# Kernel optimization log

Measured on AMD Instinct MI355X. Metric: run time of the kernel, lower is better.

The kernel has to match this reference:

```python
import jax, jax.numpy as jnp
import numpy as np
from jax import lax

N = 2048
P = 256
F_J = 0.05      # sparsity of recurrent matrix J
F_OUT = 0.05    # sparsity of readout
DT = 0.1
ON_TIME = 10
T = 200


def _activation(x):
    # Tanh_shifted_and_scaled: rates in [0, 1]
    return 0.5 * (1.0 + jnp.tanh(x))


def setup_inputs() -> dict:
    key = jax.random.key(0)
    k1, k2, k3, k4, k5 = jax.random.split(key, 5)
    # patterns ~ Uniform(-1, 1), shape [N, P]
    patterns = jax.random.uniform(k1, (N, P), jnp.float32, -1.0, 1.0)
    # sparse recurrent matrix J: gaussian values, density F_J, gain g
    g = 10.0 * 0.1 ** 0.25 / np.sqrt(N * P * np.sqrt(F_J))
    J_dense = jax.random.normal(k2, (N, N), jnp.float32) * jnp.float32(g)
    mask = jax.random.uniform(k3, (N, N)) < F_J
    J = jnp.where(mask, J_dense, 0.0).astype(jnp.float32)
    # sparse readout: ones at a random F_OUT fraction of units (frozen)
    w_out = (jax.random.uniform(k4, (N,)) < F_OUT).astype(jnp.float32)
    return {"patterns": patterns, "J": J, "w_out": w_out, "N_time_steps": T}


def reference(patterns, J, w_out, N_time_steps):
    # Batched over all P patterns at once (columns of [N, P] state).
    n = patterns.shape[0]
    x0 = jnp.zeros_like(patterns)           # [N, P]
    r0 = _activation(x0)

    def step(carry, ti):
        x, rates = carry
        inp = jnp.where(ti < ON_TIME, patterns, 0.0)      # [N, P]
        x = x + DT * (-x + J @ rates + inp)               # [N, P]
        rates = _activation(x)
        out_t = w_out @ rates                             # [P]
        return (x, rates), out_t

    _, outs = lax.scan(step, (x0, r0), jnp.arange(N_time_steps))  # [T, P]
    readout = outs.T / n                                   # [P, T]
    return readout
```

## Files before the change

kernel.cpp:

```cpp
#include <hip/hip_runtime.h>
#include <hip/hip_bf16.h>


#define NN 2048
#define PP 256
#define PAD 256
#define DT_C 0.1f
#define ON_TIME_C 10

__global__ void build_ell_kernel(const float* __restrict__ J,
                                 float2* __restrict__ ell,
                                 int* __restrict__ nnz) {
    int row  = blockIdx.x * (blockDim.x >> 6) + (threadIdx.x >> 6);
    int lane = threadIdx.x & 63;
    if (row >= NN) return;
    const float* Jrow = J + (size_t)row * NN;
    int base = 0;
    for (int c = 0; c < NN / 64; ++c) {
        float f = Jrow[c * 64 + lane];
        bool nz = (f != 0.0f);
        unsigned long long m = __ballot(nz);
        int pre = __popcll(m & ((1ull << lane) - 1ull));
        int pos = base + pre;
        if (nz && pos < PAD)
            ell[(size_t)row * PAD + pos] = make_float2(f, __int_as_float(c * 64 + lane));
        base += __popcll(m);
    }
    if (lane == 0) nnz[row] = (base < PAD) ? base : PAD;
}

__global__ void init_kernel(float* __restrict__ x, float* __restrict__ r,
                            float* __restrict__ out, int nout) {
    int i = blockIdx.x * blockDim.x + threadIdx.x;
    x[i] = 0.0f;
    r[i] = 0.5f;
    if (i < nout) out[i] = 0.0f;
}

__global__ __launch_bounds__(256) void step_kernel(
    const float2* __restrict__ ell, const int* __restrict__ nnz,
    const float* __restrict__ rates_in, float* __restrict__ rates_out,
    float* __restrict__ x, const float* __restrict__ patterns,
    const float* __restrict__ w_out, float* __restrict__ out,
    int t, int T, int with_input) {
    int row  = blockIdx.x;
    int tid  = threadIdx.x;
    int w    = tid >> 6;
    int lane = tid & 63;

    __shared__ float2 s_ell[PAD];
    __shared__ float  s_part[4][PP];

    int cnt = nnz[row];
    if (tid < cnt) s_ell[tid] = ell[(size_t)row * PAD + tid];
    __syncthreads();

    const float4* rin4 = (const float4*)rates_in;
    float4 acc = make_float4(0.f, 0.f, 0.f, 0.f);
    #pragma unroll 4
    for (int k = w; k < cnt; k += 4) {
        float2 e = s_ell[k];
        int   j  = __float_as_int(e.y);
        float4 rv = rin4[j * (PP / 4) + lane];
        acc.x = fmaf(e.x, rv.x, acc.x);
        acc.y = fmaf(e.x, rv.y, acc.y);
        acc.z = fmaf(e.x, rv.z, acc.z);
        acc.w = fmaf(e.x, rv.w, acc.w);
    }
    ((float4*)s_part[w])[lane] = acc;
    __syncthreads();

    float sum = s_part[0][tid] + s_part[1][tid] + s_part[2][tid] + s_part[3][tid];

    size_t off = (size_t)row * PP + tid;
    float xv  = x[off];
    float inp = with_input ? patterns[off] : 0.0f;
    xv += DT_C * (sum + inp - xv);
    x[off] = xv;
    float r = 0.5f * (1.0f + tanhf(xv));
    rates_out[off] = r;

    if (w_out[row] != 0.0f) {
        atomicAdd(&out[(size_t)tid * T + t], r * (1.0f / (float)NN));
    }
}

extern "C" void kernel_launch(void* const* d_in, const int* in_sizes, int n_in,
                              void* d_out, int out_size, void* d_ws, size_t ws_size,
                              hipStream_t stream) {
    const float* patterns = (const float*)d_in[0];
    const float* J        = (const float*)d_in[1];
    const float* w_out    = (const float*)d_in[2];
    float* out            = (float*)d_out;

    const int T = out_size / PP;

    size_t off = 0;
    auto alloc = [&](size_t bytes) {
        void* p = (char*)d_ws + off;
        off += (bytes + 255) & ~(size_t)255;
        return p;
    };
    float2* ell  = (float2*)alloc((size_t)NN * PAD * 8);
    int*    nnz  = (int*)   alloc((size_t)NN * 4);
    float*  x    = (float*) alloc((size_t)NN * PP * 4);
    float*  r0   = (float*) alloc((size_t)NN * PP * 4);
    float*  r1   = (float*) alloc((size_t)NN * PP * 4);
    (void)ws_size; (void)n_in; (void)in_sizes;

    build_ell_kernel<<<NN / 4, 256, 0, stream>>>(J, ell, nnz);

    init_kernel<<<(NN * PP) / 256, 256, 0, stream>>>(x, r0, out, PP * T);

    for (int t = 0; t < T; ++t) {
        const float* rin = (t & 1) ? r1 : r0;
        float*      rout = (t & 1) ? r0 : r1;
        step_kernel<<<NN, PP, 0, stream>>>(ell, nnz, rin, rout, x, patterns,
                                           w_out, out, t, T,
                                           (t < ON_TIME_C) ? 1 : 0);
    }
}
```

Before: 2.353 ms.

## Assign one wavefront per row and unroll sparse gather eightfold

```diff
diff --git a/kernel.cpp b/kernel.cpp
--- a/kernel.cpp
+++ b/kernel.cpp
@@ -37,51 +37,85 @@
     if (i < nout) out[i] = 0.0f;
 }
 
-__global__ __launch_bounds__(256) void step_kernel(
+__global__ __launch_bounds__(256, 2) void step_kernel(
     const float2* __restrict__ ell, const int* __restrict__ nnz,
     const float* __restrict__ rates_in, float* __restrict__ rates_out,
     float* __restrict__ x, const float* __restrict__ patterns,
     const float* __restrict__ w_out, float* __restrict__ out,
     int t, int T, int with_input) {
-    int row  = blockIdx.x;
-    int tid  = threadIdx.x;
-    int w    = tid >> 6;
-    int lane = tid & 63;
+    int w    = threadIdx.x >> 6;
+    int lane = threadIdx.x & 63;
+    int row  = blockIdx.x * 4 + w;
 
-    __shared__ float2 s_ell[PAD];
-    __shared__ float  s_part[4][PP];
+    __shared__ float2 s_ell[4][PAD];
 
     int cnt = nnz[row];
-    if (tid < cnt) s_ell[tid] = ell[(size_t)row * PAD + tid];
-    __syncthreads();
+    const float2* erow = ell + (size_t)row * PAD;
+    for (int i = lane; i < cnt; i += 64)
+        s_ell[w][i] = erow[i];
 
     const float4* rin4 = (const float4*)rates_in;
     float4 acc = make_float4(0.f, 0.f, 0.f, 0.f);
-    #pragma unroll 4
-    for (int k = w; k < cnt; k += 4) {
-        float2 e = s_ell[k];
-        int   j  = __float_as_int(e.y);
-        float4 rv = rin4[j * (PP / 4) + lane];
+    int k = 0;
+    for (; k + 8 <= cnt; k += 8) {
+        float2 e[8];
+        float4 rv[8];
+        #pragma unroll
+        for (int u = 0; u < 8; ++u) e[u] = s_ell[w][k + u];
+        #pragma unroll
+        for (int u = 0; u < 8; ++u)
+            rv[u] = rin4[__float_as_int(e[u].y) * (PP / 4) + lane];
+        #pragma unroll
+        for (int u = 0; u < 8; ++u) {
+            acc.x = fmaf(e[u].x, rv[u].x, acc.x);
+            acc.y = fmaf(e[u].x, rv[u].y, acc.y);
+            acc.z = fmaf(e[u].x, rv[u].z, acc.z);
+            acc.w = fmaf(e[u].x, rv[u].w, acc.w);
+        }
+    }
+    for (; k < cnt; ++k) {
+        float2 e = s_ell[w][k];
+        float4 rv = rin4[__float_as_int(e.y) * (PP / 4) + lane];
         acc.x = fmaf(e.x, rv.x, acc.x);
         acc.y = fmaf(e.x, rv.y, acc.y);
         acc.z = fmaf(e.x, rv.z, acc.z);
         acc.w = fmaf(e.x, rv.w, acc.w);
     }
-    ((float4*)s_part[w])[lane] = acc;
-    __syncthreads();
 
-    float sum = s_part[0][tid] + s_part[1][tid] + s_part[2][tid] + s_part[3][tid];
+    size_t off4 = (size_t)row * (PP / 4) + lane;
+    float4* x4        = (float4*)x;
+    float4* rout4     = (float4*)rates_out;
+    const float4* p4  = (const float4*)patterns;
 
-    size_t off = (size_t)row * PP + tid;
-    float xv  = x[off];
-    float inp = with_input ? patterns[off] : 0.0f;
-    xv += DT_C * (sum + inp - xv);
-    x[off] = xv;
-    float r = 0.5f * (1.0f + tanhf(xv));
-    rates_out[off] = r;
+    float4 xv = x4[off4];
+    if (with_input) {
+        float4 pv = p4[off4];
+        xv.x += DT_C * (acc.x + pv.x - xv.x);
+        xv.y += DT_C * (acc.y + pv.y - xv.y);
+        xv.z += DT_C * (acc.z + pv.z - xv.z);
+        xv.w += DT_C * (acc.w + pv.w - xv.w);
+    } else {
+        xv.x += DT_C * (acc.x - xv.x);
+        xv.y += DT_C * (acc.y - xv.y);
+        xv.z += DT_C * (acc.z - xv.z);
+        xv.w += DT_C * (acc.w - xv.w);
+    }
+    x4[off4] = xv;
+
+    float4 r;
+    r.x = 0.5f * (1.0f + tanhf(xv.x));
+    r.y = 0.5f * (1.0f + tanhf(xv.y));
+    r.z = 0.5f * (1.0f + tanhf(xv.z));
+    r.w = 0.5f * (1.0f + tanhf(xv.w));
+    rout4[off4] = r;
 
     if (w_out[row] != 0.0f) {
-        atomicAdd(&out[(size_t)tid * T + t], r * (1.0f / (float)NN));
+        const float s = 1.0f / (float)NN;
+        int p = lane * 4;
+        atomicAdd(&out[(size_t)(p + 0) * T + t], r.x * s);
+        atomicAdd(&out[(size_t)(p + 1) * T + t], r.y * s);
+        atomicAdd(&out[(size_t)(p + 2) * T + t], r.z * s);
+        atomicAdd(&out[(size_t)(p + 3) * T + t], r.w * s);
     }
 }
 
@@ -93,7 +127,7 @@
     const float* w_out    = (const float*)d_in[2];
     float* out            = (float*)d_out;
 
-    const int T = out_size / PP;
+    int T = out_size / PP;
 
     size_t off = 0;
     auto alloc = [&](size_t bytes) {
@@ -101,22 +135,21 @@
         off += (bytes + 255) & ~(size_t)255;
         return p;
     };
-    float2* ell  = (float2*)alloc((size_t)NN * PAD * 8);
-    int*    nnz  = (int*)   alloc((size_t)NN * 4);
-    float*  x    = (float*) alloc((size_t)NN * PP * 4);
-    float*  r0   = (float*) alloc((size_t)NN * PP * 4);
-    float*  r1   = (float*) alloc((size_t)NN * PP * 4);
+    float2* ell = (float2*)alloc((size_t)NN * PAD * 8);
+    int*    nnz = (int*)   alloc((size_t)NN * 4);
+    float*  x   = (float*) alloc((size_t)NN * PP * 4);
+    float*  r0  = (float*) alloc((size_t)NN * PP * 4);
+    float*  r1  = (float*) alloc((size_t)NN * PP * 4);
     (void)ws_size; (void)n_in; (void)in_sizes;
 
     build_ell_kernel<<<NN / 4, 256, 0, stream>>>(J, ell, nnz);
-
     init_kernel<<<(NN * PP) / 256, 256, 0, stream>>>(x, r0, out, PP * T);
 
     for (int t = 0; t < T; ++t) {
         const float* rin = (t & 1) ? r1 : r0;
         float*      rout = (t & 1) ? r0 : r1;
-        step_kernel<<<NN, PP, 0, stream>>>(ell, nnz, rin, rout, x, patterns,
-                                           w_out, out, t, T,
-                                           (t < ON_TIME_C) ? 1 : 0);
+        step_kernel<<<NN / 4, 256, 0, stream>>>(ell, nnz, rin, rout, x,
+                                                patterns, w_out, out, t, T,
+                                                (t < ON_TIME_C) ? 1 : 0);
     }
 }
```

New measurement: 2.825 ms. +20.0%, slower.

## Tile sparse matmul over K-chunks with rates staged in shared memory

Applied to the files above, without the earlier changes.

```diff
diff --git a/kernel.cpp b/kernel.cpp
--- a/kernel.cpp
+++ b/kernel.cpp
@@ -7,6 +7,11 @@
 #define PAD 256
 #define DT_C 0.1f
 #define ON_TIME_C 10
+#define KT 512
+#define NT 4
+#define MB 128
+#define CT 16
+#define SR_STRIDE 5
 
 __global__ void build_ell_kernel(const float* __restrict__ J,
                                  float2* __restrict__ ell,
@@ -29,6 +34,22 @@
     if (lane == 0) nnz[row] = (base < PAD) ? base : PAD;
 }
 
+__global__ void seg_kernel(const float2* __restrict__ ell,
+                           const int* __restrict__ nnz,
+                           int* __restrict__ seg) {
+    int r = blockIdx.x * blockDim.x + threadIdx.x;
+    if (r >= NN) return;
+    int cnt = nnz[r];
+    const float2* eb = ell + (size_t)r * PAD;
+    int tt = 0;
+    seg[r * (NT + 1)] = 0;
+    for (int i = 0; i < cnt; ++i) {
+        int k = __float_as_int(eb[i].y);
+        while (k >= (tt + 1) * KT) { ++tt; seg[r * (NT + 1) + tt] = i; }
+    }
+    while (tt < NT) { ++tt; seg[r * (NT + 1) + tt] = cnt; }
+}
+
 __global__ void init_kernel(float* __restrict__ x, float* __restrict__ r,
                             float* __restrict__ out, int nout) {
     int i = blockIdx.x * blockDim.x + threadIdx.x;
@@ -37,51 +58,114 @@
     if (i < nout) out[i] = 0.0f;
 }
 
-__global__ __launch_bounds__(256) void step_kernel(
-    const float2* __restrict__ ell, const int* __restrict__ nnz,
+__global__ __launch_bounds__(512) void step_kernel(
+    const float2* __restrict__ ell, const int* __restrict__ seg,
     const float* __restrict__ rates_in, float* __restrict__ rates_out,
     float* __restrict__ x, const float* __restrict__ patterns,
     const float* __restrict__ w_out, float* __restrict__ out,
     int t, int T, int with_input) {
-    int row  = blockIdx.x;
     int tid  = threadIdx.x;
-    int w    = tid >> 6;
-    int lane = tid & 63;
-
-    __shared__ float2 s_ell[PAD];
-    __shared__ float  s_part[4][PP];
-
-    int cnt = nnz[row];
-    if (tid < cnt) s_ell[tid] = ell[(size_t)row * PAD + tid];
+    int rt   = blockIdx.x >> 4;
+    int ct   = blockIdx.x & 15;
+    int rloc = tid >> 2;
+    int cq   = tid & 3;
+    int row  = rt * MB + rloc;
+    int cb4  = ct * (CT / 4);
+
+    __shared__ float4 sr4[KT * SR_STRIDE];
+
+    const float4* rin4 = (const float4*)rates_in;
+    const float2* eb   = ell + (size_t)row * PAD;
+
+    int sg[NT + 1];
+    #pragma unroll
+    for (int i = 0; i <= NT; ++i) sg[i] = seg[row * (NT + 1) + i];
+
+    float4 acc = make_float4(0.f, 0.f, 0.f, 0.f);
+    float4 gA, gB, gC, gD;
+
+    {
+        const float4* p = rin4 + ((size_t)(0 * KT + tid) * (PP / 4) + cb4);
+        gA = p[0]; gB = p[1]; gC = p[2]; gD = p[3];
+        sr4[tid * SR_STRIDE + 0] = gA;
+        sr4[tid * SR_STRIDE + 1] = gB;
+        sr4[tid * SR_STRIDE + 2] = gC;
+        sr4[tid * SR_STRIDE + 3] = gD;
+    }
+    {
+        const float4* p = rin4 + ((size_t)(1 * KT + tid) * (PP / 4) + cb4);
+        gA = p[0]; gB = p[1]; gC = p[2]; gD = p[3];
+    }
     __syncthreads();
 
-    const float4* rin4 = (const float4*)rates_in;
-    float4 acc = make_float4(0.f, 0.f, 0.f, 0.f);
-    #pragma unroll 4
-    for (int k = w; k < cnt; k += 4) {
-        float2 e = s_ell[k];
-        int   j  = __float_as_int(e.y);
-        float4 rv = rin4[j * (PP / 4) + lane];
-        acc.x = fmaf(e.x, rv.x, acc.x);
-        acc.y = fmaf(e.x, rv.y, acc.y);
-        acc.z = fmaf(e.x, rv.z, acc.z);
-        acc.w = fmaf(e.x, rv.w, acc.w);
-    }
-    ((float4*)s_part[w])[lane] = acc;
-    __syncthreads();
-
-    float sum = s_part[0][tid] + s_part[1][tid] + s_part[2][tid] + s_part[3][tid];
-
-    size_t off = (size_t)row * PP + tid;
-    float xv  = x[off];
-    float inp = with_input ? patterns[off] : 0.0f;
-    xv += DT_C * (sum + inp - xv);
-    x[off] = xv;
-    float r = 0.5f * (1.0f + tanhf(xv));
-    rates_out[off] = r;
+    #pragma unroll
+    for (int tt = 0; tt < NT; ++tt) {
+        int s0 = sg[tt], s1 = sg[tt + 1], kb = tt * KT;
+        float2 eA[8], eB[8];
+        #pragma unroll
+        for (int u = 0; u < 8; ++u) {
+            int i = s0 + u;
+            eA[u] = (i < s1) ? eb[i] : make_float2(0.f, __int_as_float(kb));
+        }
+        for (int i0 = s0; i0 < s1; i0 += 8) {
+            #pragma unroll
+            for (int u = 0; u < 8; ++u) {
+                int i = i0 + 8 + u;
+                eB[u] = (i < s1) ? eb[i] : make_float2(0.f, __int_as_float(kb));
+            }
+            #pragma unroll
+            for (int u = 0; u < 8; ++u) {
+                int kl = __float_as_int(eA[u].y) - kb;
+                float4 rv = sr4[kl * SR_STRIDE + cq];
+                acc.x = fmaf(eA[u].x, rv.x, acc.x);
+                acc.y = fmaf(eA[u].x, rv.y, acc.y);
+                acc.z = fmaf(eA[u].x, rv.z, acc.z);
+                acc.w = fmaf(eA[u].x, rv.w, acc.w);
+            }
+            #pragma unroll
+            for (int u = 0; u < 8; ++u) eA[u] = eB[u];
+        }
+        if (tt < NT - 1) {
+            __syncthreads();
+            sr4[tid * SR_STRIDE + 0] = gA;
+            sr4[tid * SR_STRIDE + 1] = gB;
+            sr4[tid * SR_STRIDE + 2] = gC;
+            sr4[tid * SR_STRIDE + 3] = gD;
+            if (tt < NT - 2) {
+                const float4* p = rin4 + ((size_t)((tt + 2) * KT + tid) * (PP / 4) + cb4);
+                gA = p[0]; gB = p[1]; gC = p[2]; gD = p[3];
+            }
+            __syncthreads();
+        }
+    }
+
+    size_t o4 = (size_t)row * (PP / 4) + cb4 + cq;
+    float4 xv = ((const float4*)x)[o4];
+    float4 a  = acc;
+    if (with_input) {
+        float4 pv = ((const float4*)patterns)[o4];
+        a.x += pv.x; a.y += pv.y; a.z += pv.z; a.w += pv.w;
+    }
+    xv.x += DT_C * (a.x - xv.x);
+    xv.y += DT_C * (a.y - xv.y);
+    xv.z += DT_C * (a.z - xv.z);
+    xv.w += DT_C * (a.w - xv.w);
+    ((float4*)x)[o4] = xv;
+
+    float4 r4;
+    r4.x = 0.5f * (1.0f + tanhf(xv.x));
+    r4.y = 0.5f * (1.0f + tanhf(xv.y));
+    r4.z = 0.5f * (1.0f + tanhf(xv.z));
+    r4.w = 0.5f * (1.0f + tanhf(xv.w));
+    ((float4*)rates_out)[o4] = r4;
 
     if (w_out[row] != 0.0f) {
-        atomicAdd(&out[(size_t)tid * T + t], r * (1.0f / (float)NN));
+        const float s = 1.0f / (float)NN;
+        int p0 = ct * CT + cq * 4;
+        atomicAdd(&out[(size_t)(p0 + 0) * T + t], r4.x * s);
+        atomicAdd(&out[(size_t)(p0 + 1) * T + t], r4.y * s);
+        atomicAdd(&out[(size_t)(p0 + 2) * T + t], r4.z * s);
+        atomicAdd(&out[(size_t)(p0 + 3) * T + t], r4.w * s);
     }
 }
 
@@ -93,7 +177,7 @@
     const float* w_out    = (const float*)d_in[2];
     float* out            = (float*)d_out;
 
-    const int T = out_size / PP;
+    int T = out_size / PP;
 
     size_t off = 0;
     auto alloc = [&](size_t bytes) {
@@ -101,22 +185,23 @@
         off += (bytes + 255) & ~(size_t)255;
         return p;
     };
-    float2* ell  = (float2*)alloc((size_t)NN * PAD * 8);
-    int*    nnz  = (int*)   alloc((size_t)NN * 4);
-    float*  x    = (float*) alloc((size_t)NN * PP * 4);
-    float*  r0   = (float*) alloc((size_t)NN * PP * 4);
-    float*  r1   = (float*) alloc((size_t)NN * PP * 4);
+    float2* ell = (float2*)alloc((size_t)NN * PAD * 8);
+    int*    nnz = (int*)   alloc((size_t)NN * 4);
+    int*    seg = (int*)   alloc((size_t)NN * (NT + 1) * 4);
+    float*  x   = (float*) alloc((size_t)NN * PP * 4);
+    float*  r0  = (float*) alloc((size_t)NN * PP * 4);
+    float*  r1  = (float*) alloc((size_t)NN * PP * 4);
     (void)ws_size; (void)n_in; (void)in_sizes;
 
     build_ell_kernel<<<NN / 4, 256, 0, stream>>>(J, ell, nnz);
-
+    seg_kernel<<<NN / 256, 256, 0, stream>>>(ell, nnz, seg);
     init_kernel<<<(NN * PP) / 256, 256, 0, stream>>>(x, r0, out, PP * T);
 
     for (int t = 0; t < T; ++t) {
         const float* rin = (t & 1) ? r1 : r0;
         float*      rout = (t & 1) ? r0 : r1;
-        step_kernel<<<NN, PP, 0, stream>>>(ell, nnz, rin, rout, x, patterns,
-                                           w_out, out, t, T,
-                                           (t < ON_TIME_C) ? 1 : 0);
-    }
-}
+        step_kernel<<<256, 512, 0, stream>>>(ell, seg, rin, rout, x, patterns,
+                                             w_out, out, t, T,
+                                             (t < ON_TIME_C) ? 1 : 0);
+    }
+}
```

New measurement: 4.436 ms. 1.89x slower.
